# Optimization experiments

Hardware: AMD Instinct MI355X
Metric: run time of the kernel (lower is better)

## Reference

```python
import jax, jax.numpy as jnp
import numpy as np

B, D, K, H, L = 8192, 512, 64, 256, 3  # batch, hidden width, rank_k, hypernet hidden, n layers


def _xavier(key, shape):
    fan_in, fan_out = shape[0], shape[1]
    std = float(np.sqrt(2.0 / (fan_in + fan_out)))
    return jax.random.normal(key, shape, dtype=jnp.float32) * std


def setup_inputs() -> dict:
    key = jax.random.key(0)
    ks = jax.random.split(key, 32)
    inp = {"x": jax.random.normal(ks[0], (B, D), dtype=jnp.float32)}
    i = 1
    for l in range(1, L + 1):
        inp[f"U{l}"] = _xavier(ks[i], (D, K)); i += 1
        inp[f"V{l}"] = _xavier(ks[i], (K, D)); i += 1
        # hypernet: cond_dim D -> H -> (K*K + D) [first D cols are bias]
        inp[f"hW1_{l}"] = _xavier(ks[i], (D, H)); i += 1
        inp[f"hb1_{l}"] = jnp.zeros((H,), dtype=jnp.float32)
        inp[f"hW2_{l}"] = _xavier(ks[i], (H, K * K + D)); i += 1
        inp[f"hb2_{l}"] = jnp.zeros((K * K + D,), dtype=jnp.float32)
    inp["Wout"] = _xavier(ks[i], (D, 1)); i += 1
    inp["bout"] = jnp.zeros((1,), dtype=jnp.float32)
    return inp


def _apg_layer(x, U, V, hW1, hb1, hW2, hb2):
    # hypernet (self-wise: condition_z = x)
    h1 = jax.nn.relu(x @ hW1 + hb1)            # [B, H]
    s = h1 @ hW2 + hb2                          # [B, K*K + D]
    bias = s[:, :D]                             # generated per-sample bias [B, D]
    S = s[:, D:].reshape(-1, K, K)              # per-sample weight [B, K, K]
    h = x @ U                                   # [B, K]
    h = jnp.einsum('bk,bkj->bj', h, S)          # bmm(h.unsqueeze(1), S).squeeze(1)
    out = h @ V + bias                          # [B, D]
    return jax.nn.relu(out)


def reference(x,
              U1, V1, hW1_1, hb1_1, hW2_1, hb2_1,
              U2, V2, hW1_2, hb1_2, hW2_2, hb2_2,
              U3, V3, hW1_3, hb1_3, hW2_3, hb2_3,
              Wout, bout):
    x = _apg_layer(x, U1, V1, hW1_1, hb1_1, hW2_1, hb2_1)
    x = _apg_layer(x, U2, V2, hW1_2, hb1_2, hW2_2, hb2_2)
    x = _apg_layer(x, U3, V3, hW1_3, hb1_3, hW2_3, hb2_3)
    return x @ Wout + bout                      # [B, 1]
```

## Files before the change

kernel.cpp:

```cpp
#include <hip/hip_runtime.h>

#define B_N 8192
#define D_N 512
#define K_N 64
#define H_N 256
#define SC  4608
#define R_T 32
#define NT  512

typedef __attribute__((ext_vector_type(8))) short short8;
typedef __attribute__((ext_vector_type(4))) short short4v;
typedef __attribute__((ext_vector_type(4))) float f32x4;

__device__ __forceinline__ unsigned short f2bf(float f) {
  unsigned int u = __builtin_bit_cast(unsigned int, f);
  u += 0x7fff + ((u >> 16) & 1);
  return (unsigned short)(u >> 16);
}
__device__ __forceinline__ float bf2f(unsigned short h) {
  unsigned int u = ((unsigned int)h) << 16;
  return __builtin_bit_cast(float, u);
}

#define L_ELEMS 1376256

struct PrepParams {
  const float* W1[3]; const float* U[3]; const float* W2[3]; const float* V[3];
  short* ws;
};

__global__ __launch_bounds__(256) void prep_weights(PrepParams p) {
  const int y = blockIdx.y;
  const int l = y / 5, m = y - 5 * l;
  short* wsl = p.ws + (size_t)l * L_ELEMS;
  if (m == 2) {
    const float* in = p.W2[l];
    short* out = wsl + 163840;
    const long total = 1048576;
    for (long e = (long)blockIdx.x * 256 + threadIdx.x; e < total;
         e += (long)gridDim.x * 256) {
      const int te   = (int)(e & 7);
      const int lane = (int)((e >> 3) & 63);
      const int kk   = (int)((e >> 9) & 3);
      const int nq   = (int)((e >> 11) & 3);
      const int h2   = (int)((e >> 13) & 1);
      const int kg   = (int)(e >> 14);
      const int g    = lane >> 4;
      const int l15  = lane & 15;
      const int t    = h2 * 128 + kk * 32 + g * 8 + te;
      out[e] = (short)f2bf(in[(size_t)t * SC + 512 + 64 * kg + nq * 16 + l15]);
    }
    return;
  }
  const float* in; short* out; int K, istride, ioff, kshift;
  switch (m) {
    case 0: in = p.W1[l]; out = wsl;           K = 512; istride = 256;  ioff = 0; kshift = 9; break;
    case 1: in = p.U[l];  out = wsl + 131072;  K = 512; istride = 64;   ioff = 0; kshift = 9; break;
    case 3: in = p.W2[l]; out = wsl + 1212416; K = 256; istride = 4608; ioff = 0; kshift = 8; break;
    default:in = p.V[l];  out = wsl + 1343488; K = 64;  istride = 512;  ioff = 0; kshift = 6; break;
  }
  const long total = (long)K * ((m == 0) ? 256 : (m == 1) ? 64 : 512);
  for (long e = (long)blockIdx.x * 256 + threadIdx.x; e < total;
       e += (long)gridDim.x * 256) {
    const int k = (int)(e & (K - 1));
    const int n = (int)(e >> kshift);
    out[e] = (short)f2bf(in[(size_t)k * istride + ioff + n]);
  }
}

struct Params {
  const float* x;
  const float* b1[3];
  const float* b2[3];
  const float* Wout;
  const float* bout;
  const short* ws;
  float* out;
};

#define XP 520
#define HP 264
#define TP 72

__device__ __forceinline__ void stage_chunk(const short* W2p, short* slotp,
                                            int cglob, int nq, int lane) {
  const short* gp = W2p + (((size_t)cglob * 4 + nq) << 11) + (lane << 3);
#pragma unroll
  for (int i = 0; i < 4; ++i) {
    __builtin_amdgcn_global_load_lds(
        (const __attribute__((address_space(1))) void*)(gp + (i << 9)),
        (__attribute__((address_space(3))) void*)(slotp + (i << 9)), 16, 0, 0);
  }
}

__global__ __launch_bounds__(NT, 1) void apg_mfma(Params p) {
  __shared__ __attribute__((aligned(16))) short ring[8][3][2048];
  __shared__ short h1s[R_T][HP];
  __shared__ short tmps[R_T][TP];
  __shared__ float hs[R_T][68];
  __shared__ float tpart[R_T][68];
  short (*xs)[XP] = (short (*)[XP]) & ring[0][0][0];

  const int tid  = threadIdx.x;
  const int row0 = blockIdx.x * R_T;
  const int w    = tid >> 6;
  const int lane = tid & 63;
  const int l15  = tid & 15;
  const int g    = (tid & 63) >> 4;
  const int koff = g * 8;
  const int rh   = w >> 2;
  const int nq   = w & 3;
  const int rbase = rh * 16;

  {
    const float4* xg = (const float4*)(p.x + (size_t)row0 * D_N);
    for (int i = tid; i < R_T * D_N / 4; i += NT) {
      float4 v = xg[i];
      const int r = i >> 7;
      const int c = (i & 127) << 2;
      short4v s4 = { (short)f2bf(v.x), (short)f2bf(v.y), (short)f2bf(v.z), (short)f2bf(v.w) };
      *(short4v*)&xs[r][c] = s4;
    }
  }
  __syncthreads();

  for (int l = 0; l < 3; ++l) {
    const short* wsl  = p.ws + (size_t)l * L_ELEMS;
    const short* W1T  = wsl;
    const short* UT   = wsl + 131072;
    const short* W2p  = wsl + 163840;
    const short* W2bT = wsl + 1212416;
    const short* VT   = wsl + 1343488;
    const float* b1 = p.b1[l];
    const float* b2 = p.b2[l];

    short8 aX[16];
#pragma unroll
    for (int kk = 0; kk < 16; ++kk)
      aX[kk] = *(const short8*)&xs[rbase + l15][kk * 32 + koff];

    for (int nf = 0; nf < 4; ++nf) {
      const int n0 = ((nq << 2) + nf) << 4;
      const short* pb = W1T + ((size_t)(n0 + l15) << 9) + koff;
      short8 bf[16];
#pragma unroll
      for (int kk = 0; kk < 16; ++kk) bf[kk] = *(const short8*)(pb + kk * 32);
      f32x4 acc = {0.f, 0.f, 0.f, 0.f};
#pragma unroll
      for (int kk = 0; kk < 16; ++kk)
        acc = __builtin_amdgcn_mfma_f32_16x16x32_bf16(aX[kk], bf[kk], acc, 0, 0, 0);
      const float bb = b1[n0 + l15];
#pragma unroll
      for (int i = 0; i < 4; ++i)
        h1s[rbase + g * 4 + i][n0 + l15] = (short)f2bf(fmaxf(acc[i] + bb, 0.f));
    }

    {
      const int n0 = nq << 4;
      const short* pb = UT + ((size_t)(n0 + l15) << 9) + koff;
      short8 bf[16];
#pragma unroll
      for (int kk = 0; kk < 16; ++kk) bf[kk] = *(const short8*)(pb + kk * 32);
      f32x4 acc = {0.f, 0.f, 0.f, 0.f};
#pragma unroll
      for (int kk = 0; kk < 16; ++kk)
        acc = __builtin_amdgcn_mfma_f32_16x16x32_bf16(aX[kk], bf[kk], acc, 0, 0, 0);
#pragma unroll
      for (int i = 0; i < 4; ++i) hs[rbase + g * 4 + i][n0 + l15] = acc[i];
    }
    __syncthreads();

    {
      const int kh  = w >> 2;
      const int kg0 = kh << 5;
      const int nl  = (nq << 4) + l15;
      short8 aH0[8], aH1[8];
#pragma unroll
      for (int kk = 0; kk < 8; ++kk) {
        aH0[kk] = *(const short8*)&h1s[l15][kk * 32 + koff];
        aH1[kk] = *(const short8*)&h1s[16 + l15][kk * 32 + koff];
      }
      float t0[4] = {0.f, 0.f, 0.f, 0.f}, t1[4] = {0.f, 0.f, 0.f, 0.f};
      {
        const float* pb2 = b2 + D_N + nl;
#pragma unroll 4
        for (int k = kg0; k < kg0 + 32; ++k) {
          const float b2v = pb2[k << 6];
#pragma unroll
          for (int i = 0; i < 4; ++i) {
            t0[i] += hs[g * 4 + i][k] * b2v;
            t1[i] += hs[16 + g * 4 + i][k] * b2v;
          }
        }
      }

      short* ringw = &ring[w][0][0];
      const int cbase = kg0 << 1;

      asm volatile("s_waitcnt vmcnt(0)" ::: "memory");
      stage_chunk(W2p, ringw,        cbase + 0, nq, lane);
      stage_chunk(W2p, ringw + 2048, cbase + 1, nq, lane);
      stage_chunk(W2p, ringw + 4096, cbase + 2, nq, lane);

#pragma unroll 1
      for (int kgi = 0; kgi < 32; ++kgi) {
        const int kg = kg0 + kgi;
        f32x4 s0 = {0.f, 0.f, 0.f, 0.f}, s1 = {0.f, 0.f, 0.f, 0.f};
        {
          const int slot = (2 * kgi) % 3;
          if (kgi < 31) asm volatile("s_waitcnt vmcnt(8)" ::: "memory");
          else          asm volatile("s_waitcnt vmcnt(4)" ::: "memory");
          const short* rb = ringw + slot * 2048 + (lane << 3);
          short8 bf[4];
#pragma unroll
          for (int kk = 0; kk < 4; ++kk) bf[kk] = *(const short8*)(rb + (kk << 9));
          asm volatile("s_waitcnt lgkmcnt(0)" ::: "memory");
          __builtin_amdgcn_sched_barrier(0);
          if (kgi <= 30)
            stage_chunk(W2p, ringw + slot * 2048, cbase + 2 * kgi + 3, nq, lane);
#pragma unroll
          for (int kk = 0; kk < 4; ++kk) {
            s0 = __builtin_amdgcn_mfma_f32_16x16x32_bf16(aH0[kk], bf[kk], s0, 0, 0, 0);
            s1 = __builtin_amdgcn_mfma_f32_16x16x32_bf16(aH1[kk], bf[kk], s1, 0, 0, 0);
          }
        }
        {
          const int slot = (2 * kgi + 1) % 3;
          if (kgi < 31) asm volatile("s_waitcnt vmcnt(8)" ::: "memory");
          else          asm volatile("s_waitcnt vmcnt(0)" ::: "memory");
          const short* rb = ringw + slot * 2048 + (lane << 3);
          short8 bf[4];
#pragma unroll
          for (int kk = 0; kk < 4; ++kk) bf[kk] = *(const short8*)(rb + (kk << 9));
          asm volatile("s_waitcnt lgkmcnt(0)" ::: "memory");
          __builtin_amdgcn_sched_barrier(0);
          if (kgi <= 29)
            stage_chunk(W2p, ringw + slot * 2048, cbase + 2 * kgi + 4, nq, lane);
#pragma unroll
          for (int kk = 0; kk < 4; ++kk) {
            s0 = __builtin_amdgcn_mfma_f32_16x16x32_bf16(aH0[4 + kk], bf[kk], s0, 0, 0, 0);
            s1 = __builtin_amdgcn_mfma_f32_16x16x32_bf16(aH1[4 + kk], bf[kk], s1, 0, 0, 0);
          }
        }
#pragma unroll
        for (int i = 0; i < 4; ++i) {
          t0[i] += hs[g * 4 + i][kg] * s0[i];
          t1[i] += hs[16 + g * 4 + i][kg] * s1[i];
        }
      }

      if (kh == 0) {
#pragma unroll
        for (int i = 0; i < 4; ++i) {
          tpart[g * 4 + i][nl]      = t0[i];
          tpart[16 + g * 4 + i][nl] = t1[i];
        }
      }
      __syncthreads();
      if (kh == 1) {
#pragma unroll
        for (int i = 0; i < 4; ++i) {
          tmps[g * 4 + i][nl]      = (short)f2bf(tpart[g * 4 + i][nl] + t0[i]);
          tmps[16 + g * 4 + i][nl] = (short)f2bf(tpart[16 + g * 4 + i][nl] + t1[i]);
        }
      }
    }
    __syncthreads();

    {
      short8 aT[2], aD[8];
#pragma unroll
      for (int kk = 0; kk < 2; ++kk)
        aT[kk] = *(const short8*)&tmps[rbase + l15][kk * 32 + koff];
#pragma unroll
      for (int kk = 0; kk < 8; ++kk)
        aD[kk] = *(const short8*)&h1s[rbase + l15][kk * 32 + koff];
      for (int ti = 0; ti < 8; ++ti) {
        const int n0 = ((ti << 2) + nq) << 4;
        const short* pv = VT + ((size_t)(n0 + l15) << 6) + koff;
        const short* pw = W2bT + ((size_t)(n0 + l15) << 8) + koff;
        short8 bv[2], bw[8];
#pragma unroll
        for (int kk = 0; kk < 2; ++kk) bv[kk] = *(const short8*)(pv + kk * 32);
#pragma unroll
        for (int kk = 0; kk < 8; ++kk) bw[kk] = *(const short8*)(pw + kk * 32);
        f32x4 acc = {0.f, 0.f, 0.f, 0.f};
#pragma unroll
        for (int kk = 0; kk < 2; ++kk)
          acc = __builtin_amdgcn_mfma_f32_16x16x32_bf16(aT[kk], bv[kk], acc, 0, 0, 0);
#pragma unroll
        for (int kk = 0; kk < 8; ++kk)
          acc = __builtin_amdgcn_mfma_f32_16x16x32_bf16(aD[kk], bw[kk], acc, 0, 0, 0);
        const float bb = b2[n0 + l15];
#pragma unroll
        for (int i = 0; i < 4; ++i)
          xs[rbase + g * 4 + i][n0 + l15] = (short)f2bf(fmaxf(acc[i] + bb, 0.f));
      }
    }
    __syncthreads();
  }

  {
    const int r  = tid >> 4;
    const int cl = tid & 15;
    float acc = 0.f;
    for (int c = cl; c < D_N; c += 16)
      acc = fmaf(bf2f((unsigned short)xs[r][c]), p.Wout[c], acc);
#pragma unroll
    for (int s = 1; s < 16; s <<= 1) acc += __shfl_xor(acc, s, 64);
    if (cl == 0) p.out[row0 + r] = acc + p.bout[0];
  }
}

extern "C" void kernel_launch(void* const* d_in, const int* in_sizes, int n_in,
                              void* d_out, int out_size, void* d_ws, size_t ws_size,
                              hipStream_t stream) {
  (void)in_sizes; (void)n_in; (void)ws_size; (void)out_size;
  PrepParams pp;
  Params p;
  p.x = (const float*)d_in[0];
  for (int l = 0; l < 3; ++l) {
    const int base = 1 + l * 6;
    pp.U[l]  = (const float*)d_in[base + 0];
    pp.V[l]  = (const float*)d_in[base + 1];
    pp.W1[l] = (const float*)d_in[base + 2];
    p.b1[l]  = (const float*)d_in[base + 3];
    pp.W2[l] = (const float*)d_in[base + 4];
    p.b2[l]  = (const float*)d_in[base + 5];
  }
  p.Wout = (const float*)d_in[19];
  p.bout = (const float*)d_in[20];
  p.ws   = (const short*)d_ws;
  p.out  = (float*)d_out;
  pp.ws  = (short*)d_ws;

  hipLaunchKernelGGL(prep_weights, dim3(1024, 15), dim3(256), 0, stream, pp);
  hipLaunchKernelGGL(apg_mfma, dim3(B_N / R_T), dim3(NT), 0, stream, p);
}
```

Before: 216.3 us.

## Split fused APG layer kernel into per-stage kernels with workspace intermediates

Replaces the single fused per-row-tile kernel with a multi-kernel pipeline per layer: one kernel computes h1 and x@U, one computes the per-sample einsum with 64-row tiles split across two blocks per tile and combined by atomicAdd into a zeroed fp32 buffer, and one computes the V projection plus generated bias, with a final output kernel. Intermediates go through global workspace instead of LDS, and the W2 weight layout is repacked for the new einsum tiling. The intent is to raise parallelism and weight reuse in the dominant einsum stage, at the cost of extra launches, memsets, global round-trips and atomics. The old fused path is kept as a fallback when the workspace is too small.

```diff
diff --git a/kernel.cpp b/kernel.cpp
--- a/kernel.cpp
+++ b/kernel.cpp
@@ -5,7 +5,6 @@
 #define K_N 64
 #define H_N 256
 #define SC  4608
-#define R_T 32
 #define NT  512
 
 typedef __attribute__((ext_vector_type(8))) short short8;
@@ -24,12 +23,262 @@
 
 #define L_ELEMS 1376256
 
+#define OFF_H1  8257536u
+#define OFF_H   12451840u
+#define OFF_TMP 14548992u
+#define OFF_X   16646144u
+#define WS_NEED 25034752u
+
 struct PrepParams {
   const float* W1[3]; const float* U[3]; const float* W2[3]; const float* V[3];
   short* ws;
 };
 
-__global__ __launch_bounds__(256) void prep_weights(PrepParams p) {
+__global__ __launch_bounds__(256) void prep_main(PrepParams p) {
+  const int y = blockIdx.y;
+  const int l = y / 5, m = y - 5 * l;
+  short* wsl = p.ws + (size_t)l * L_ELEMS;
+  if (m == 2) {
+    const float* in = p.W2[l];
+    short* out = wsl + 163840;
+    const long total = 1048576;
+    for (long e = (long)blockIdx.x * 256 + threadIdx.x; e < total;
+         e += (long)gridDim.x * 256) {
+      const int te   = (int)(e & 7);
+      const int lane = (int)((e >> 3) & 63);
+      const int cf   = (int)((e >> 9) & 3);
+      const int ks   = (int)((e >> 11) & 7);
+      const int kg   = (int)(e >> 14);
+      const int t    = ks * 32 + (lane >> 4) * 8 + te;
+      const int j    = cf * 16 + (lane & 15);
+      out[e] = (short)f2bf(in[(size_t)t * SC + 512 + 64 * kg + j]);
+    }
+    return;
+  }
+  const float* in; short* out; int K, istride, ioff, kshift;
+  switch (m) {
+    case 0: in = p.W1[l]; out = wsl;           K = 512; istride = 256;  ioff = 0; kshift = 9; break;
+    case 1: in = p.U[l];  out = wsl + 131072;  K = 512; istride = 64;   ioff = 0; kshift = 9; break;
+    case 3: in = p.W2[l]; out = wsl + 1212416; K = 256; istride = 4608; ioff = 0; kshift = 8; break;
+    default:in = p.V[l];  out = wsl + 1343488; K = 64;  istride = 512;  ioff = 0; kshift = 6; break;
+  }
+  const long total = (long)K * ((m == 0) ? 256 : (m == 1) ? 64 : 512);
+  for (long e = (long)blockIdx.x * 256 + threadIdx.x; e < total;
+       e += (long)gridDim.x * 256) {
+    const int k = (int)(e & (K - 1));
+    const int n = (int)(e >> kshift);
+    out[e] = (short)f2bf(in[(size_t)k * istride + ioff + n]);
+  }
+}
+
+struct K1Params {
+  const float* xf;
+  const short* xb;
+  const short* wsl;
+  const float* b1;
+  short* h1w; float* hw;
+};
+__global__ __launch_bounds__(NT, 1) void k1_h1h(K1Params p) {
+  __shared__ short xs[32][520];
+  const int tid = threadIdx.x;
+  const int w = tid >> 6, rh = w >> 2, nq = w & 3;
+  const int l15 = tid & 15, g = (tid & 63) >> 4, koff = g * 8;
+  const int R0 = blockIdx.x * 32, rbase = rh * 16;
+
+  if (p.xf) {
+    const float4* xg = (const float4*)(p.xf + (size_t)R0 * D_N);
+    for (int i = tid; i < 32 * D_N / 4; i += NT) {
+      float4 v = xg[i];
+      const int r = i >> 7, c = (i & 127) << 2;
+      short4v s4 = { (short)f2bf(v.x), (short)f2bf(v.y), (short)f2bf(v.z), (short)f2bf(v.w) };
+      *(short4v*)&xs[r][c] = s4;
+    }
+  } else {
+    const short8* xg = (const short8*)(p.xb + (size_t)R0 * D_N);
+    for (int i = tid; i < 32 * D_N / 8; i += NT) {
+      short8 v = xg[i];
+      const int r = i >> 6, c = (i & 63) << 3;
+      *(short8*)&xs[r][c] = v;
+    }
+  }
+  __syncthreads();
+
+  short8 aX[16];
+#pragma unroll
+  for (int kk = 0; kk < 16; ++kk)
+    aX[kk] = *(const short8*)&xs[rbase + l15][kk * 32 + koff];
+
+  for (int f = 0; f < 5; ++f) {
+    const int n0 = nq * 80 + f * 16;
+    const bool ish1 = (n0 < 256);
+    const short* pb = ish1 ? (p.wsl + ((size_t)(n0 + l15) << 9) + koff)
+                           : (p.wsl + 131072 + ((size_t)(n0 - 256 + l15) << 9) + koff);
+    short8 bf[16];
+#pragma unroll
+    for (int kk = 0; kk < 16; ++kk) bf[kk] = *(const short8*)(pb + kk * 32);
+    f32x4 acc = {0.f, 0.f, 0.f, 0.f};
+#pragma unroll
+    for (int kk = 0; kk < 16; ++kk)
+      acc = __builtin_amdgcn_mfma_f32_16x16x32_bf16(aX[kk], bf[kk], acc, 0, 0, 0);
+    if (ish1) {
+      const float bb = p.b1[n0 + l15];
+#pragma unroll
+      for (int i = 0; i < 4; ++i)
+        p.h1w[(size_t)(R0 + rbase + g * 4 + i) * 256 + n0 + l15] =
+            (short)f2bf(fmaxf(acc[i] + bb, 0.f));
+    } else {
+#pragma unroll
+      for (int i = 0; i < 4; ++i)
+        p.hw[(size_t)(R0 + rbase + g * 4 + i) * 64 + (n0 - 256) + l15] = acc[i];
+    }
+  }
+}
+
+struct K2Params {
+  const short* w2k; const short* h1w; const float* hw;
+  const float* b2; float* tmpf;
+};
+__global__ __launch_bounds__(NT, 1) void k2_einsum(K2Params p) {
+  __shared__ float tpartL[4][64][68];
+  const int tid = threadIdx.x;
+  const int w = tid >> 6, lane = tid & 63;
+  const int l15 = tid & 15, g = (tid & 63) >> 4, koff = g * 8;
+  const int rt = blockIdx.x >> 1, kh = blockIdx.x & 1;
+  const int R0 = rt * 64;
+  const int m2 = w >> 2, s = w & 3;
+  const int rb = m2 * 32;
+  const int kgbase = kh * 32 + s * 8;
+
+  short8 aH0[8], aH1[8];
+#pragma unroll
+  for (int kk = 0; kk < 8; ++kk) {
+    aH0[kk] = *(const short8*)&p.h1w[(size_t)(R0 + rb + l15) * 256 + kk * 32 + koff];
+    aH1[kk] = *(const short8*)&p.h1w[(size_t)(R0 + rb + 16 + l15) * 256 + kk * 32 + koff];
+  }
+  float ta0[4][4] = {{0.f}}, ta1[4][4] = {{0.f}};
+
+#pragma unroll 1
+  for (int q = 0; q < 8; ++q) {
+    const int kg = kgbase + q;
+    const short* bbase = p.w2k + ((size_t)kg << 14) + (lane << 3);
+    f32x4 s0[4], s1[4];
+#pragma unroll
+    for (int cf = 0; cf < 4; ++cf) {
+      f32x4 z = {0.f, 0.f, 0.f, 0.f};
+      s0[cf] = z; s1[cf] = z;
+    }
+#pragma unroll
+    for (int h2 = 0; h2 < 2; ++h2) {
+      short8 bf[16];
+#pragma unroll
+      for (int kw = 0; kw < 4; ++kw)
+#pragma unroll
+        for (int cf = 0; cf < 4; ++cf)
+          bf[kw * 4 + cf] = *(const short8*)(bbase + ((((h2 * 4 + kw) * 4 + cf)) << 9));
+#pragma unroll
+      for (int kw = 0; kw < 4; ++kw)
+#pragma unroll
+        for (int cf = 0; cf < 4; ++cf) {
+          s0[cf] = __builtin_amdgcn_mfma_f32_16x16x32_bf16(aH0[h2 * 4 + kw], bf[kw * 4 + cf], s0[cf], 0, 0, 0);
+          s1[cf] = __builtin_amdgcn_mfma_f32_16x16x32_bf16(aH1[h2 * 4 + kw], bf[kw * 4 + cf], s1[cf], 0, 0, 0);
+        }
+    }
+    const float* pb2 = p.b2 + D_N + (kg << 6);
+    float b2v[4];
+#pragma unroll
+    for (int cf = 0; cf < 4; ++cf) b2v[cf] = pb2[cf * 16 + l15];
+#pragma unroll
+    for (int i = 0; i < 4; ++i) {
+      const float hv0 = p.hw[(size_t)(R0 + rb + g * 4 + i) * 64 + kg];
+      const float hv1 = p.hw[(size_t)(R0 + rb + 16 + g * 4 + i) * 64 + kg];
+#pragma unroll
+      for (int cf = 0; cf < 4; ++cf) {
+        ta0[cf][i] += hv0 * (s0[cf][i] + b2v[cf]);
+        ta1[cf][i] += hv1 * (s1[cf][i] + b2v[cf]);
+      }
+    }
+  }
+
+#pragma unroll
+  for (int cf = 0; cf < 4; ++cf)
+#pragma unroll
+    for (int i = 0; i < 4; ++i) {
+      tpartL[s][rb + g * 4 + i][cf * 16 + l15]      = ta0[cf][i];
+      tpartL[s][rb + 16 + g * 4 + i][cf * 16 + l15] = ta1[cf][i];
+    }
+  __syncthreads();
+  for (int e = tid; e < 4096; e += NT) {
+    const int r = e >> 6, c = e & 63;
+    const float v = (tpartL[0][r][c] + tpartL[1][r][c]) +
+                    (tpartL[2][r][c] + tpartL[3][r][c]);
+    atomicAdd(&p.tmpf[(size_t)(R0 + r) * 64 + c], v);
+  }
+}
+
+struct K3Params {
+  const short* wsl; const short* h1w; const float* tmpf;
+  const float* b2; short* xw;
+};
+__global__ __launch_bounds__(NT, 1) void k3_proj(K3Params p) {
+  const int tid = threadIdx.x;
+  const int w = tid >> 6, rh = w >> 2, nq = w & 3;
+  const int l15 = tid & 15, g = (tid & 63) >> 4, koff = g * 8;
+  const int R0 = blockIdx.x * 32, rbase = rh * 16;
+  const short* W2bT = p.wsl + 1212416;
+  const short* VT   = p.wsl + 1343488;
+
+  short8 aT[2];
+#pragma unroll
+  for (int kk = 0; kk < 2; ++kk) {
+    short8 t;
+#pragma unroll
+    for (int e = 0; e < 8; ++e)
+      t[e] = (short)f2bf(p.tmpf[(size_t)(R0 + rbase + l15) * 64 + kk * 32 + koff + e]);
+    aT[kk] = t;
+  }
+  short8 aD[8];
+#pragma unroll
+  for (int kk = 0; kk < 8; ++kk)
+    aD[kk] = *(const short8*)&p.h1w[(size_t)(R0 + rbase + l15) * 256 + kk * 32 + koff];
+
+  for (int ti = 0; ti < 8; ++ti) {
+    const int n0 = ((ti << 2) + nq) << 4;
+    const short* pv = VT + ((size_t)(n0 + l15) << 6) + koff;
+    const short* pw = W2bT + ((size_t)(n0 + l15) << 8) + koff;
+    short8 bv[2], bw[8];
+#pragma unroll
+    for (int kk = 0; kk < 2; ++kk) bv[kk] = *(const short8*)(pv + kk * 32);
+#pragma unroll
+    for (int kk = 0; kk < 8; ++kk) bw[kk] = *(const short8*)(pw + kk * 32);
+    f32x4 acc = {0.f, 0.f, 0.f, 0.f};
+#pragma unroll
+    for (int kk = 0; kk < 2; ++kk)
+      acc = __builtin_amdgcn_mfma_f32_16x16x32_bf16(aT[kk], bv[kk], acc, 0, 0, 0);
+#pragma unroll
+    for (int kk = 0; kk < 8; ++kk)
+      acc = __builtin_amdgcn_mfma_f32_16x16x32_bf16(aD[kk], bw[kk], acc, 0, 0, 0);
+    const float bb = p.b2[n0 + l15];
+#pragma unroll
+    for (int i = 0; i < 4; ++i)
+      p.xw[(size_t)(R0 + rbase + g * 4 + i) * 512 + n0 + l15] =
+          (short)f2bf(fmaxf(acc[i] + bb, 0.f));
+  }
+}
+
+__global__ __launch_bounds__(NT, 1) void k4_out(const short* xw, const float* Wout,
+                                                const float* bout, float* out) {
+  const int tid = threadIdx.x;
+  const int R0 = blockIdx.x * 32;
+  const int r = tid >> 4, cl = tid & 15;
+  float acc = 0.f;
+  for (int c = cl; c < D_N; c += 16)
+    acc = fmaf(bf2f((unsigned short)xw[(size_t)(R0 + r) * 512 + c]), Wout[c], acc);
+#pragma unroll
+  for (int s = 1; s < 16; s <<= 1) acc += __shfl_xor(acc, s, 64);
+  if (cl == 0) out[R0 + r] = acc + bout[0];
+}
+
+__global__ __launch_bounds__(256) void prep_fb(PrepParams p) {
   const int y = blockIdx.y;
   const int l = y / 5, m = y - 5 * l;
   short* wsl = p.ws + (size_t)l * L_ELEMS;
@@ -93,16 +342,16 @@
   }
 }
 
-__global__ __launch_bounds__(NT, 1) void apg_mfma(Params p) {
+__global__ __launch_bounds__(NT, 1) void apg_fb(Params p) {
   __shared__ __attribute__((aligned(16))) short ring[8][3][2048];
-  __shared__ short h1s[R_T][HP];
-  __shared__ short tmps[R_T][TP];
-  __shared__ float hs[R_T][68];
-  __shared__ float tpart[R_T][68];
+  __shared__ short h1s[32][HP];
+  __shared__ short tmps[32][TP];
+  __shared__ float hs[32][68];
+  __shared__ float tpart[32][68];
   short (*xs)[XP] = (short (*)[XP]) & ring[0][0][0];
 
   const int tid  = threadIdx.x;
-  const int row0 = blockIdx.x * R_T;
+  const int row0 = blockIdx.x * 32;
   const int w    = tid >> 6;
   const int lane = tid & 63;
   const int l15  = tid & 15;
@@ -114,7 +363,7 @@
 
   {
     const float4* xg = (const float4*)(p.x + (size_t)row0 * D_N);
-    for (int i = tid; i < R_T * D_N / 4; i += NT) {
+    for (int i = tid; i < 32 * D_N / 4; i += NT) {
       float4 v = xg[i];
       const int r = i >> 7;
       const int c = (i & 127) << 2;
@@ -315,25 +564,61 @@
 extern "C" void kernel_launch(void* const* d_in, const int* in_sizes, int n_in,
                               void* d_out, int out_size, void* d_ws, size_t ws_size,
                               hipStream_t stream) {
-  (void)in_sizes; (void)n_in; (void)ws_size; (void)out_size;
+  (void)in_sizes; (void)n_in; (void)out_size;
   PrepParams pp;
-  Params p;
-  p.x = (const float*)d_in[0];
+  const float* xf = (const float*)d_in[0];
+  const float* b1p[3]; const float* b2p[3];
   for (int l = 0; l < 3; ++l) {
     const int base = 1 + l * 6;
     pp.U[l]  = (const float*)d_in[base + 0];
     pp.V[l]  = (const float*)d_in[base + 1];
     pp.W1[l] = (const float*)d_in[base + 2];
-    p.b1[l]  = (const float*)d_in[base + 3];
+    b1p[l]   = (const float*)d_in[base + 3];
     pp.W2[l] = (const float*)d_in[base + 4];
-    p.b2[l]  = (const float*)d_in[base + 5];
-  }
-  p.Wout = (const float*)d_in[19];
-  p.bout = (const float*)d_in[20];
-  p.ws   = (const short*)d_ws;
-  p.out  = (float*)d_out;
-  pp.ws  = (short*)d_ws;
-
-  hipLaunchKernelGGL(prep_weights, dim3(1024, 15), dim3(256), 0, stream, pp);
-  hipLaunchKernelGGL(apg_mfma, dim3(B_N / R_T), dim3(NT), 0, stream, p);
-}
+    b2p[l]   = (const float*)d_in[base + 5];
+  }
+  const float* Wout = (const float*)d_in[19];
+  const float* bout = (const float*)d_in[20];
+  pp.ws = (short*)d_ws;
+
+  if (ws_size >= (size_t)WS_NEED) {
+    short* wsw  = (short*)d_ws;
+    short* h1w  = (short*)((char*)d_ws + OFF_H1);
+    float* hw   = (float*)((char*)d_ws + OFF_H);
+    float* tmpf = (float*)((char*)d_ws + OFF_TMP);
+    short* xw   = (short*)((char*)d_ws + OFF_X);
+
+    hipLaunchKernelGGL(prep_main, dim3(1024, 15), dim3(256), 0, stream, pp);
+    for (int l = 0; l < 3; ++l) {
+      K1Params p1;
+      p1.xf = (l == 0) ? xf : nullptr;
+      p1.xb = xw;
+      p1.wsl = wsw + (size_t)l * L_ELEMS;
+      p1.b1 = b1p[l]; p1.h1w = h1w; p1.hw = hw;
+      hipLaunchKernelGGL(k1_h1h, dim3(B_N / 32), dim3(NT), 0, stream, p1);
+
+      hipMemsetAsync(tmpf, 0, (size_t)B_N * 64 * 4, stream);
+
+      K2Params p2;
+      p2.w2k = wsw + (size_t)l * L_ELEMS + 163840;
+      p2.h1w = h1w; p2.hw = hw; p2.b2 = b2p[l]; p2.tmpf = tmpf;
+      hipLaunchKernelGGL(k2_einsum, dim3(B_N / 32), dim3(NT), 0, stream, p2);
+
+      K3Params p3;
+      p3.wsl = wsw + (size_t)l * L_ELEMS;
+      p3.h1w = h1w; p3.tmpf = tmpf; p3.b2 = b2p[l]; p3.xw = xw;
+      hipLaunchKernelGGL(k3_proj, dim3(B_N / 32), dim3(NT), 0, stream, p3);
+    }
+    hipLaunchKernelGGL(k4_out, dim3(B_N / 32), dim3(NT), 0, stream,
+                       (const short*)xw, Wout, bout, (float*)d_out);
+  } else {
+    Params p;
+    p.x = xf;
+    for (int l = 0; l < 3; ++l) { p.b1[l] = b1p[l]; p.b2[l] = b2p[l]; }
+    p.Wout = Wout; p.bout = bout;
+    p.ws = (const short*)d_ws;
+    p.out = (float*)d_out;
+    hipLaunchKernelGGL(prep_fb, dim3(1024, 15), dim3(256), 0, stream, pp);
+    hipLaunchKernelGGL(apg_fb, dim3(B_N / 32), dim3(NT), 0, stream, p);
+  }
+}
```

Result: slower. 351.1 us (+62.3%).

## Split fused APG kernel into per-layer kernels with 64-row tiles and split-K atomics

Applied to the files above, without the earlier changes.

The single fused three-layer kernel becomes three launches per layer plus a final output kernel. The hypernet stage now works on 64-row tiles, so each W2 chunk streamed into LDS is reused across four 16-row MFMA sets instead of two. The K-group dimension is split across two blocks that merge partial results with global float atomics into a zeroed buffer. The cost is extra launches and memsets, global round trips for h1, the partial results and x between kernels, and atomic traffic.

```diff
diff --git a/kernel.cpp b/kernel.cpp
--- a/kernel.cpp
+++ b/kernel.cpp
@@ -5,7 +5,6 @@
 #define K_N 64
 #define H_N 256
 #define SC  4608
-#define R_T 32
 #define NT  512
 
 typedef __attribute__((ext_vector_type(8))) short short8;
@@ -23,6 +22,10 @@
 }
 
 #define L_ELEMS 1376256
+
+#define OFF_H1  8257536u
+#define OFF_TMP 14548992u
+#define OFF_X   16646144u
 
 struct PrepParams {
   const float* W1[3]; const float* U[3]; const float* W2[3]; const float* V[3];
@@ -68,20 +71,6 @@
   }
 }
 
-struct Params {
-  const float* x;
-  const float* b1[3];
-  const float* b2[3];
-  const float* Wout;
-  const float* bout;
-  const short* ws;
-  float* out;
-};
-
-#define XP 520
-#define HP 264
-#define TP 72
-
 __device__ __forceinline__ void stage_chunk(const short* W2p, short* slotp,
                                             int cglob, int nq, int lane) {
   const short* gp = W2p + (((size_t)cglob * 4 + nq) << 11) + (lane << 3);
@@ -93,247 +82,312 @@
   }
 }
 
-__global__ __launch_bounds__(NT, 1) void apg_mfma(Params p) {
+struct PParams {
+  const float* xf;
+  const short* xb;
+  const short* wsl;
+  const float* b1;
+  const float* b2;
+  short* h1w;
+  float* tmpf;
+};
+
+__global__ __launch_bounds__(NT, 1) void apg_p(PParams p) {
   __shared__ __attribute__((aligned(16))) short ring[8][3][2048];
-  __shared__ short h1s[R_T][HP];
-  __shared__ short tmps[R_T][TP];
-  __shared__ float hs[R_T][68];
-  __shared__ float tpart[R_T][68];
-  short (*xs)[XP] = (short (*)[XP]) & ring[0][0][0];
+  __shared__ short h1s[64][264];
+  __shared__ float hs[64][68];
+  short (*xs)[520] = (short (*)[520]) & ring[0][0][0];
 
   const int tid  = threadIdx.x;
-  const int row0 = blockIdx.x * R_T;
   const int w    = tid >> 6;
   const int lane = tid & 63;
   const int l15  = tid & 15;
   const int g    = (tid & 63) >> 4;
   const int koff = g * 8;
-  const int rh   = w >> 2;
   const int nq   = w & 3;
-  const int rbase = rh * 16;
-
-  {
-    const float4* xg = (const float4*)(p.x + (size_t)row0 * D_N);
-    for (int i = tid; i < R_T * D_N / 4; i += NT) {
+  const int rt   = blockIdx.x >> 1;
+  const int kh   = blockIdx.x & 1;
+  const int R0   = rt * 64;
+
+  if (p.xf) {
+    const float4* xg = (const float4*)(p.xf + (size_t)R0 * D_N);
+    for (int i = tid; i < 64 * D_N / 4; i += NT) {
       float4 v = xg[i];
-      const int r = i >> 7;
-      const int c = (i & 127) << 2;
+      const int r = i >> 7, c = (i & 127) << 2;
       short4v s4 = { (short)f2bf(v.x), (short)f2bf(v.y), (short)f2bf(v.z), (short)f2bf(v.w) };
       *(short4v*)&xs[r][c] = s4;
     }
+  } else {
+    const short8* xg = (const short8*)(p.xb + (size_t)R0 * D_N);
+    for (int i = tid; i < 64 * D_N / 8; i += NT) {
+      short8 v = xg[i];
+      const int r = i >> 6, c = (i & 63) << 3;
+      *(short8*)&xs[r][c] = v;
+    }
   }
   __syncthreads();
 
-  for (int l = 0; l < 3; ++l) {
-    const short* wsl  = p.ws + (size_t)l * L_ELEMS;
-    const short* W1T  = wsl;
-    const short* UT   = wsl + 131072;
-    const short* W2p  = wsl + 163840;
-    const short* W2bT = wsl + 1212416;
-    const short* VT   = wsl + 1343488;
-    const float* b1 = p.b1[l];
-    const float* b2 = p.b2[l];
-
-    short8 aX[16];
-#pragma unroll
-    for (int kk = 0; kk < 16; ++kk)
-      aX[kk] = *(const short8*)&xs[rbase + l15][kk * 32 + koff];
-
-    for (int nf = 0; nf < 4; ++nf) {
-      const int n0 = ((nq << 2) + nf) << 4;
-      const short* pb = W1T + ((size_t)(n0 + l15) << 9) + koff;
-      short8 bf[16];
-#pragma unroll
-      for (int kk = 0; kk < 16; ++kk) bf[kk] = *(const short8*)(pb + kk * 32);
-      f32x4 acc = {0.f, 0.f, 0.f, 0.f};
+  {
+    const int rh2 = w >> 2;
+    for (int rs = 0; rs < 2; ++rs) {
+      const int rb = rh2 * 32 + rs * 16;
+      short8 aX[16];
 #pragma unroll
       for (int kk = 0; kk < 16; ++kk)
-        acc = __builtin_amdgcn_mfma_f32_16x16x32_bf16(aX[kk], bf[kk], acc, 0, 0, 0);
-      const float bb = b1[n0 + l15];
-#pragma unroll
-      for (int i = 0; i < 4; ++i)
-        h1s[rbase + g * 4 + i][n0 + l15] = (short)f2bf(fmaxf(acc[i] + bb, 0.f));
-    }
-
+        aX[kk] = *(const short8*)&xs[rb + l15][kk * 32 + koff];
+      for (int f = 0; f < 5; ++f) {
+        const int n0 = nq * 80 + f * 16;
+        const bool ish1 = (n0 < 256);
+        const short* pb = ish1 ? (p.wsl + ((size_t)(n0 + l15) << 9) + koff)
+                               : (p.wsl + 131072 + ((size_t)(n0 - 256 + l15) << 9) + koff);
+        short8 bf[16];
+#pragma unroll
+        for (int kk = 0; kk < 16; ++kk) bf[kk] = *(const short8*)(pb + kk * 32);
+        f32x4 acc = {0.f, 0.f, 0.f, 0.f};
+#pragma unroll
+        for (int kk = 0; kk < 16; ++kk)
+          acc = __builtin_amdgcn_mfma_f32_16x16x32_bf16(aX[kk], bf[kk], acc, 0, 0, 0);
+        if (ish1) {
+          const float bb = p.b1[n0 + l15];
+#pragma unroll
+          for (int i = 0; i < 4; ++i) {
+            const short v = (short)f2bf(fmaxf(acc[i] + bb, 0.f));
+            h1s[rb + g * 4 + i][n0 + l15] = v;
+            if (kh == 0)
+              p.h1w[(size_t)(R0 + rb + g * 4 + i) * 256 + n0 + l15] = v;
+          }
+        } else {
+#pragma unroll
+          for (int i = 0; i < 4; ++i)
+            hs[rb + g * 4 + i][n0 - 256 + l15] = acc[i];
+        }
+      }
+    }
+  }
+  __syncthreads();
+
+  {
+    const short* W2p = p.wsl + 163840;
+    const int kq   = w >> 2;
+    const int kg0w = kh * 32 + kq * 16;
+    const int nl   = nq * 16 + l15;
+    float t[4][4];
+#pragma unroll
+    for (int rset = 0; rset < 4; ++rset)
+#pragma unroll
+      for (int i = 0; i < 4; ++i) t[rset][i] = 0.f;
     {
-      const int n0 = nq << 4;
-      const short* pb = UT + ((size_t)(n0 + l15) << 9) + koff;
-      short8 bf[16];
-#pragma unroll
-      for (int kk = 0; kk < 16; ++kk) bf[kk] = *(const short8*)(pb + kk * 32);
-      f32x4 acc = {0.f, 0.f, 0.f, 0.f};
-#pragma unroll
-      for (int kk = 0; kk < 16; ++kk)
-        acc = __builtin_amdgcn_mfma_f32_16x16x32_bf16(aX[kk], bf[kk], acc, 0, 0, 0);
-#pragma unroll
-      for (int i = 0; i < 4; ++i) hs[rbase + g * 4 + i][n0 + l15] = acc[i];
+      const float* pb2 = p.b2 + D_N + nl;
+#pragma unroll 4
+      for (int k = kg0w; k < kg0w + 16; ++k) {
+        const float b2v = pb2[k << 6];
+#pragma unroll
+        for (int rset = 0; rset < 4; ++rset)
+#pragma unroll
+          for (int i = 0; i < 4; ++i)
+            t[rset][i] += hs[rset * 16 + g * 4 + i][k] * b2v;
+      }
+    }
+
+    short* ringw = &ring[w][0][0];
+    const int cbase = kg0w << 1;
+
+    asm volatile("s_waitcnt vmcnt(0)" ::: "memory");
+    stage_chunk(W2p, ringw,        cbase + 0, nq, lane);
+    stage_chunk(W2p, ringw + 2048, cbase + 1, nq, lane);
+    stage_chunk(W2p, ringw + 4096, cbase + 2, nq, lane);
+
+#pragma unroll 1
+    for (int kgi = 0; kgi < 16; ++kgi) {
+      const int kg = kg0w + kgi;
+      f32x4 s[4];
+#pragma unroll
+      for (int rset = 0; rset < 4; ++rset) {
+        f32x4 z = {0.f, 0.f, 0.f, 0.f};
+        s[rset] = z;
+      }
+      {
+        const int slot = (2 * kgi) % 3;
+        if (kgi < 15) asm volatile("s_waitcnt vmcnt(8)" ::: "memory");
+        else          asm volatile("s_waitcnt vmcnt(4)" ::: "memory");
+        const short* rb = ringw + slot * 2048 + (lane << 3);
+        short8 bf[4];
+#pragma unroll
+        for (int kk = 0; kk < 4; ++kk) bf[kk] = *(const short8*)(rb + (kk << 9));
+        short8 aHt[4][4];
+#pragma unroll
+        for (int rset = 0; rset < 4; ++rset)
+#pragma unroll
+          for (int kk = 0; kk < 4; ++kk)
+            aHt[rset][kk] = *(const short8*)&h1s[rset * 16 + l15][kk * 32 + koff];
+        asm volatile("s_waitcnt lgkmcnt(0)" ::: "memory");
+        __builtin_amdgcn_sched_barrier(0);
+        if (2 * kgi + 3 <= 31)
+          stage_chunk(W2p, ringw + slot * 2048, cbase + 2 * kgi + 3, nq, lane);
+#pragma unroll
+        for (int kk = 0; kk < 4; ++kk)
+#pragma unroll
+          for (int rset = 0; rset < 4; ++rset)
+            s[rset] = __builtin_amdgcn_mfma_f32_16x16x32_bf16(aHt[rset][kk], bf[kk], s[rset], 0, 0, 0);
+      }
+      {
+        const int slot = (2 * kgi + 1) % 3;
+        if (kgi < 15) asm volatile("s_waitcnt vmcnt(8)" ::: "memory");
+        else          asm volatile("s_waitcnt vmcnt(0)" ::: "memory");
+        const short* rb = ringw + slot * 2048 + (lane << 3);
+        short8 bf[4];
+#pragma unroll
+        for (int kk = 0; kk < 4; ++kk) bf[kk] = *(const short8*)(rb + (kk << 9));
+        short8 aHt[4][4];
+#pragma unroll
+        for (int rset = 0; rset < 4; ++rset)
+#pragma unroll
+          for (int kk = 0; kk < 4; ++kk)
+            aHt[rset][kk] = *(const short8*)&h1s[rset * 16 + l15][(4 + kk) * 32 + koff];
+        asm volatile("s_waitcnt lgkmcnt(0)" ::: "memory");
+        __builtin_amdgcn_sched_barrier(0);
+        if (2 * kgi + 4 <= 31)
+          stage_chunk(W2p, ringw + slot * 2048, cbase + 2 * kgi + 4, nq, lane);
+#pragma unroll
+        for (int kk = 0; kk < 4; ++kk)
+#pragma unroll
+          for (int rset = 0; rset < 4; ++rset)
+            s[rset] = __builtin_amdgcn_mfma_f32_16x16x32_bf16(aHt[rset][kk], bf[kk], s[rset], 0, 0, 0);
+      }
+#pragma unroll
+      for (int rset = 0; rset < 4; ++rset)
+#pragma unroll
+        for (int i = 0; i < 4; ++i)
+          t[rset][i] += hs[rset * 16 + g * 4 + i][kg] * s[rset][i];
+    }
+
+    float* tpw = (float*)&ring[w][0][0];
+    if (kq == 0) {
+#pragma unroll
+      for (int rset = 0; rset < 4; ++rset)
+#pragma unroll
+        for (int i = 0; i < 4; ++i)
+          tpw[(rset * 16 + g * 4 + i) * 16 + l15] = t[rset][i];
     }
     __syncthreads();
-
-    {
-      const int kh  = w >> 2;
-      const int kg0 = kh << 5;
-      const int nl  = (nq << 4) + l15;
-      short8 aH0[8], aH1[8];
-#pragma unroll
-      for (int kk = 0; kk < 8; ++kk) {
-        aH0[kk] = *(const short8*)&h1s[l15][kk * 32 + koff];
-        aH1[kk] = *(const short8*)&h1s[16 + l15][kk * 32 + koff];
-      }
-      float t0[4] = {0.f, 0.f, 0.f, 0.f}, t1[4] = {0.f, 0.f, 0.f, 0.f};
-      {
-        const float* pb2 = b2 + D_N + nl;
-#pragma unroll 4
-        for (int k = kg0; k < kg0 + 32; ++k) {
-          const float b2v = pb2[k << 6];
-#pragma unroll
-          for (int i = 0; i < 4; ++i) {
-            t0[i] += hs[g * 4 + i][k] * b2v;
-            t1[i] += hs[16 + g * 4 + i][k] * b2v;
-          }
+    if (kq == 1) {
+      const float* tpp = (const float*)&ring[nq][0][0];
+#pragma unroll
+      for (int rset = 0; rset < 4; ++rset)
+#pragma unroll
+        for (int i = 0; i < 4; ++i) {
+          const int row = rset * 16 + g * 4 + i;
+          const float v = tpp[row * 16 + l15] + t[rset][i];
+          atomicAdd(&p.tmpf[(size_t)(R0 + row) * 64 + nl], v);
         }
-      }
-
-      short* ringw = &ring[w][0][0];
-      const int cbase = kg0 << 1;
-
-      asm volatile("s_waitcnt vmcnt(0)" ::: "memory");
-      stage_chunk(W2p, ringw,        cbase + 0, nq, lane);
-      stage_chunk(W2p, ringw + 2048, cbase + 1, nq, lane);
-      stage_chunk(W2p, ringw + 4096, cbase + 2, nq, lane);
-
-#pragma unroll 1
-      for (int kgi = 0; kgi < 32; ++kgi) {
-        const int kg = kg0 + kgi;
-        f32x4 s0 = {0.f, 0.f, 0.f, 0.f}, s1 = {0.f, 0.f, 0.f, 0.f};
-        {
-          const int slot = (2 * kgi) % 3;
-          if (kgi < 31) asm volatile("s_waitcnt vmcnt(8)" ::: "memory");
-          else          asm volatile("s_waitcnt vmcnt(4)" ::: "memory");
-          const short* rb = ringw + slot * 2048 + (lane << 3);
-          short8 bf[4];
-#pragma unroll
-          for (int kk = 0; kk < 4; ++kk) bf[kk] = *(const short8*)(rb + (kk << 9));
-          asm volatile("s_waitcnt lgkmcnt(0)" ::: "memory");
-          __builtin_amdgcn_sched_barrier(0);
-          if (kgi <= 30)
-            stage_chunk(W2p, ringw + slot * 2048, cbase + 2 * kgi + 3, nq, lane);
-#pragma unroll
-          for (int kk = 0; kk < 4; ++kk) {
-            s0 = __builtin_amdgcn_mfma_f32_16x16x32_bf16(aH0[kk], bf[kk], s0, 0, 0, 0);
-            s1 = __builtin_amdgcn_mfma_f32_16x16x32_bf16(aH1[kk], bf[kk], s1, 0, 0, 0);
-          }
-        }
-        {
-          const int slot = (2 * kgi + 1) % 3;
-          if (kgi < 31) asm volatile("s_waitcnt vmcnt(8)" ::: "memory");
-          else          asm volatile("s_waitcnt vmcnt(0)" ::: "memory");
-          const short* rb = ringw + slot * 2048 + (lane << 3);
-          short8 bf[4];
-#pragma unroll
-          for (int kk = 0; kk < 4; ++kk) bf[kk] = *(const short8*)(rb + (kk << 9));
-          asm volatile("s_waitcnt lgkmcnt(0)" ::: "memory");
-          __builtin_amdgcn_sched_barrier(0);
-          if (kgi <= 29)
-            stage_chunk(W2p, ringw + slot * 2048, cbase + 2 * kgi + 4, nq, lane);
-#pragma unroll
-          for (int kk = 0; kk < 4; ++kk) {
-            s0 = __builtin_amdgcn_mfma_f32_16x16x32_bf16(aH0[4 + kk], bf[kk], s0, 0, 0, 0);
-            s1 = __builtin_amdgcn_mfma_f32_16x16x32_bf16(aH1[4 + kk], bf[kk], s1, 0, 0, 0);
-          }
-        }
-#pragma unroll
-        for (int i = 0; i < 4; ++i) {
-          t0[i] += hs[g * 4 + i][kg] * s0[i];
-          t1[i] += hs[16 + g * 4 + i][kg] * s1[i];
-        }
-      }
-
-      if (kh == 0) {
-#pragma unroll
-        for (int i = 0; i < 4; ++i) {
-          tpart[g * 4 + i][nl]      = t0[i];
-          tpart[16 + g * 4 + i][nl] = t1[i];
-        }
-      }
-      __syncthreads();
-      if (kh == 1) {
-#pragma unroll
-        for (int i = 0; i < 4; ++i) {
-          tmps[g * 4 + i][nl]      = (short)f2bf(tpart[g * 4 + i][nl] + t0[i]);
-          tmps[16 + g * 4 + i][nl] = (short)f2bf(tpart[16 + g * 4 + i][nl] + t1[i]);
-        }
-      }
-    }
-    __syncthreads();
-
-    {
-      short8 aT[2], aD[8];
-#pragma unroll
-      for (int kk = 0; kk < 2; ++kk)
-        aT[kk] = *(const short8*)&tmps[rbase + l15][kk * 32 + koff];
-#pragma unroll
-      for (int kk = 0; kk < 8; ++kk)
-        aD[kk] = *(const short8*)&h1s[rbase + l15][kk * 32 + koff];
-      for (int ti = 0; ti < 8; ++ti) {
-        const int n0 = ((ti << 2) + nq) << 4;
-        const short* pv = VT + ((size_t)(n0 + l15) << 6) + koff;
-        const short* pw = W2bT + ((size_t)(n0 + l15) << 8) + koff;
-        short8 bv[2], bw[8];
-#pragma unroll
-        for (int kk = 0; kk < 2; ++kk) bv[kk] = *(const short8*)(pv + kk * 32);
-#pragma unroll
-        for (int kk = 0; kk < 8; ++kk) bw[kk] = *(const short8*)(pw + kk * 32);
-        f32x4 acc = {0.f, 0.f, 0.f, 0.f};
-#pragma unroll
-        for (int kk = 0; kk < 2; ++kk)
-          acc = __builtin_amdgcn_mfma_f32_16x16x32_bf16(aT[kk], bv[kk], acc, 0, 0, 0);
-#pragma unroll
-        for (int kk = 0; kk < 8; ++kk)
-          acc = __builtin_amdgcn_mfma_f32_16x16x32_bf16(aD[kk], bw[kk], acc, 0, 0, 0);
-        const float bb = b2[n0 + l15];
-#pragma unroll
-        for (int i = 0; i < 4; ++i)
-          xs[rbase + g * 4 + i][n0 + l15] = (short)f2bf(fmaxf(acc[i] + bb, 0.f));
-      }
-    }
-    __syncthreads();
-  }
-
-  {
-    const int r  = tid >> 4;
-    const int cl = tid & 15;
-    float acc = 0.f;
-    for (int c = cl; c < D_N; c += 16)
-      acc = fmaf(bf2f((unsigned short)xs[r][c]), p.Wout[c], acc);
-#pragma unroll
-    for (int s = 1; s < 16; s <<= 1) acc += __shfl_xor(acc, s, 64);
-    if (cl == 0) p.out[row0 + r] = acc + p.bout[0];
-  }
+    }
+  }
+}
+
+struct K3Params {
+  const short* wsl; const short* h1w; const float* tmpf;
+  const float* b2; short* xw;
+};
+__global__ __launch_bounds__(NT, 1) void k3_proj(K3Params p) {
+  const int tid = threadIdx.x;
+  const int w = tid >> 6, rh = w >> 2, nq = w & 3;
+  const int l15 = tid & 15, g = (tid & 63) >> 4, koff = g * 8;
+  const int R0 = blockIdx.x * 32, rbase = rh * 16;
+  const short* W2bT = p.wsl + 1212416;
+  const short* VT   = p.wsl + 1343488;
+
+  short8 aT[2];
+#pragma unroll
+  for (int kk = 0; kk < 2; ++kk) {
+    short8 t;
+#pragma unroll
+    for (int e = 0; e < 8; ++e)
+      t[e] = (short)f2bf(p.tmpf[(size_t)(R0 + rbase + l15) * 64 + kk * 32 + koff + e]);
+    aT[kk] = t;
+  }
+  short8 aD[8];
+#pragma unroll
+  for (int kk = 0; kk < 8; ++kk)
+    aD[kk] = *(const short8*)&p.h1w[(size_t)(R0 + rbase + l15) * 256 + kk * 32 + koff];
+
+  for (int ti = 0; ti < 8; ++ti) {
+    const int n0 = ((ti << 2) + nq) << 4;
+    const short* pv = VT + ((size_t)(n0 + l15) << 6) + koff;
+    const short* pw = W2bT + ((size_t)(n0 + l15) << 8) + koff;
+    short8 bv[2], bw[8];
+#pragma unroll
+    for (int kk = 0; kk < 2; ++kk) bv[kk] = *(const short8*)(pv + kk * 32);
+#pragma unroll
+    for (int kk = 0; kk < 8; ++kk) bw[kk] = *(const short8*)(pw + kk * 32);
+    f32x4 acc = {0.f, 0.f, 0.f, 0.f};
+#pragma unroll
+    for (int kk = 0; kk < 2; ++kk)
+      acc = __builtin_amdgcn_mfma_f32_16x16x32_bf16(aT[kk], bv[kk], acc, 0, 0, 0);
+#pragma unroll
+    for (int kk = 0; kk < 8; ++kk)
+      acc = __builtin_amdgcn_mfma_f32_16x16x32_bf16(aD[kk], bw[kk], acc, 0, 0, 0);
+    const float bb = p.b2[n0 + l15];
+#pragma unroll
+    for (int i = 0; i < 4; ++i)
+      p.xw[(size_t)(R0 + rbase + g * 4 + i) * 512 + n0 + l15] =
+          (short)f2bf(fmaxf(acc[i] + bb, 0.f));
+  }
+}
+
+__global__ __launch_bounds__(NT, 1) void k4_out(const short* xw, const float* Wout,
+                                                const float* bout, float* out) {
+  const int tid = threadIdx.x;
+  const int R0 = blockIdx.x * 32;
+  const int r = tid >> 4, cl = tid & 15;
+  float acc = 0.f;
+  for (int c = cl; c < D_N; c += 16)
+    acc = fmaf(bf2f((unsigned short)xw[(size_t)(R0 + r) * 512 + c]), Wout[c], acc);
+#pragma unroll
+  for (int s = 1; s < 16; s <<= 1) acc += __shfl_xor(acc, s, 64);
+  if (cl == 0) out[R0 + r] = acc + bout[0];
 }
 
 extern "C" void kernel_launch(void* const* d_in, const int* in_sizes, int n_in,
                               void* d_out, int out_size, void* d_ws, size_t ws_size,
                               hipStream_t stream) {
-  (void)in_sizes; (void)n_in; (void)ws_size; (void)out_size;
+  (void)in_sizes; (void)n_in; (void)out_size; (void)ws_size;
   PrepParams pp;
-  Params p;
-  p.x = (const float*)d_in[0];
+  const float* xf = (const float*)d_in[0];
+  const float* b1p[3]; const float* b2p[3];
   for (int l = 0; l < 3; ++l) {
     const int base = 1 + l * 6;
     pp.U[l]  = (const float*)d_in[base + 0];
     pp.V[l]  = (const float*)d_in[base + 1];
     pp.W1[l] = (const float*)d_in[base + 2];
-    p.b1[l]  = (const float*)d_in[base + 3];
+    b1p[l]   = (const float*)d_in[base + 3];
     pp.W2[l] = (const float*)d_in[base + 4];
-    p.b2[l]  = (const float*)d_in[base + 5];
-  }
-  p.Wout = (const float*)d_in[19];
-  p.bout = (const float*)d_in[20];
-  p.ws   = (const short*)d_ws;
-  p.out  = (float*)d_out;
-  pp.ws  = (short*)d_ws;
+    b2p[l]   = (const float*)d_in[base + 5];
+  }
+  const float* Wout = (const float*)d_in[19];
+  const float* bout = (const float*)d_in[20];
+  pp.ws = (short*)d_ws;
+
+  short* wsw  = (short*)d_ws;
+  short* h1w  = (short*)((char*)d_ws + OFF_H1);
+  float* tmpf = (float*)((char*)d_ws + OFF_TMP);
+  short* xw   = (short*)((char*)d_ws + OFF_X);
 
   hipLaunchKernelGGL(prep_weights, dim3(1024, 15), dim3(256), 0, stream, pp);
-  hipLaunchKernelGGL(apg_mfma, dim3(B_N / R_T), dim3(NT), 0, stream, p);
-}
+  for (int l = 0; l < 3; ++l) {
+    hipMemsetAsync(tmpf, 0, (size_t)B_N * 64 * 4, stream);
+    PParams p1;
+    p1.xf = (l == 0) ? xf : nullptr;
+    p1.xb = xw;
+    p1.wsl = wsw + (size_t)l * L_ELEMS;
+    p1.b1 = b1p[l]; p1.b2 = b2p[l];
+    p1.h1w = h1w; p1.tmpf = tmpf;
+    hipLaunchKernelGGL(apg_p, dim3(B_N / 32), dim3(NT), 0, stream, p1);
+
+    K3Params p3;
+    p3.wsl = wsw + (size_t)l * L_ELEMS;
+    p3.h1w = h1w; p3.tmpf = tmpf; p3.b2 = b2p[l]; p3.xw = xw;
+    hipLaunchKernelGGL(k3_proj, dim3(B_N / 32), dim3(NT), 0, stream, p3);
+  }
+  hipLaunchKernelGGL(k4_out, dim3(B_N / 32), dim3(NT), 0, stream,
+                     (const short*)xw, Wout, bout, (float*)d_out);
+}
```

Measured after the change: 316.0 us. 46.1% more time.

## Deepen W2 LDS ring to four slots with register double-buffered B fragments

Applied to the files above, without the earlier changes.

Grows the per-wave LDS ring from three to four chunk slots and restructures the main loop into a 4-chunk unrolled software pipeline. Each chunk's LDS reads are issued one stage ahead, into alternating register buffers, so they overlap with the MFMAs of the previous chunk instead of waiting on lgkmcnt(0). The tpart reduction buffer is removed and the ring memory is reused for the cross-wave partial sums, which offsets the LDS growth. This adds register pressure and complexity in the waitcnt accounting.

```diff
diff --git a/kernel.cpp b/kernel.cpp
--- a/kernel.cpp
+++ b/kernel.cpp
@@ -93,12 +93,45 @@
   }
 }
 
+#define DS_READ4(dst, SLOT)                                                   \
+  do {                                                                        \
+    const short* rb_ = ringw + (SLOT) * 2048 + (lane << 3);                   \
+    dst[0] = *(const short8*)(rb_);                                           \
+    dst[1] = *(const short8*)(rb_ + 512);                                     \
+    dst[2] = *(const short8*)(rb_ + 1024);                                    \
+    dst[3] = *(const short8*)(rb_ + 1536);                                    \
+  } while (0)
+
+#define MFMA_TH0(bf)                                                          \
+  do {                                                                        \
+    f32x4 z_ = {0.f, 0.f, 0.f, 0.f};                                          \
+    s0 = z_; s1 = z_;                                                         \
+    _Pragma("unroll")                                                         \
+    for (int kk = 0; kk < 4; ++kk) {                                          \
+      s0 = __builtin_amdgcn_mfma_f32_16x16x32_bf16(aH0[kk], bf[kk], s0, 0, 0, 0); \
+      s1 = __builtin_amdgcn_mfma_f32_16x16x32_bf16(aH1[kk], bf[kk], s1, 0, 0, 0); \
+    }                                                                         \
+  } while (0)
+
+#define MFMA_TH1_FOLD(bf, KG)                                                 \
+  do {                                                                        \
+    _Pragma("unroll")                                                         \
+    for (int kk = 0; kk < 4; ++kk) {                                          \
+      s0 = __builtin_amdgcn_mfma_f32_16x16x32_bf16(aH0[4 + kk], bf[kk], s0, 0, 0, 0); \
+      s1 = __builtin_amdgcn_mfma_f32_16x16x32_bf16(aH1[4 + kk], bf[kk], s1, 0, 0, 0); \
+    }                                                                         \
+    _Pragma("unroll")                                                         \
+    for (int i = 0; i < 4; ++i) {                                             \
+      t0[i] += hs[g * 4 + i][(KG)] * s0[i];                                   \
+      t1[i] += hs[16 + g * 4 + i][(KG)] * s1[i];                              \
+    }                                                                         \
+  } while (0)
+
 __global__ __launch_bounds__(NT, 1) void apg_mfma(Params p) {
-  __shared__ __attribute__((aligned(16))) short ring[8][3][2048];
+  __shared__ __attribute__((aligned(16))) short ring[8][4][2048];
   __shared__ short h1s[R_T][HP];
   __shared__ short tmps[R_T][TP];
   __shared__ float hs[R_T][68];
-  __shared__ float tpart[R_T][68];
   short (*xs)[XP] = (short (*)[XP]) & ring[0][0][0];
 
   const int tid  = threadIdx.x;
@@ -201,67 +234,76 @@
       stage_chunk(W2p, ringw,        cbase + 0, nq, lane);
       stage_chunk(W2p, ringw + 2048, cbase + 1, nq, lane);
       stage_chunk(W2p, ringw + 4096, cbase + 2, nq, lane);
+      stage_chunk(W2p, ringw + 6144, cbase + 3, nq, lane);
+      asm volatile("s_waitcnt vmcnt(12)" ::: "memory");
+      short8 bfA[4], bfB[4];
+      DS_READ4(bfA, 0);
+      f32x4 s0, s1;
 
 #pragma unroll 1
-      for (int kgi = 0; kgi < 32; ++kgi) {
-        const int kg = kg0 + kgi;
-        f32x4 s0 = {0.f, 0.f, 0.f, 0.f}, s1 = {0.f, 0.f, 0.f, 0.f};
-        {
-          const int slot = (2 * kgi) % 3;
-          if (kgi < 31) asm volatile("s_waitcnt vmcnt(8)" ::: "memory");
-          else          asm volatile("s_waitcnt vmcnt(4)" ::: "memory");
-          const short* rb = ringw + slot * 2048 + (lane << 3);
-          short8 bf[4];
-#pragma unroll
-          for (int kk = 0; kk < 4; ++kk) bf[kk] = *(const short8*)(rb + (kk << 9));
-          asm volatile("s_waitcnt lgkmcnt(0)" ::: "memory");
-          __builtin_amdgcn_sched_barrier(0);
-          if (kgi <= 30)
-            stage_chunk(W2p, ringw + slot * 2048, cbase + 2 * kgi + 3, nq, lane);
-#pragma unroll
-          for (int kk = 0; kk < 4; ++kk) {
-            s0 = __builtin_amdgcn_mfma_f32_16x16x32_bf16(aH0[kk], bf[kk], s0, 0, 0, 0);
-            s1 = __builtin_amdgcn_mfma_f32_16x16x32_bf16(aH1[kk], bf[kk], s1, 0, 0, 0);
-          }
-        }
-        {
-          const int slot = (2 * kgi + 1) % 3;
-          if (kgi < 31) asm volatile("s_waitcnt vmcnt(8)" ::: "memory");
-          else          asm volatile("s_waitcnt vmcnt(0)" ::: "memory");
-          const short* rb = ringw + slot * 2048 + (lane << 3);
-          short8 bf[4];
-#pragma unroll
-          for (int kk = 0; kk < 4; ++kk) bf[kk] = *(const short8*)(rb + (kk << 9));
-          asm volatile("s_waitcnt lgkmcnt(0)" ::: "memory");
-          __builtin_amdgcn_sched_barrier(0);
-          if (kgi <= 29)
-            stage_chunk(W2p, ringw + slot * 2048, cbase + 2 * kgi + 4, nq, lane);
-#pragma unroll
-          for (int kk = 0; kk < 4; ++kk) {
-            s0 = __builtin_amdgcn_mfma_f32_16x16x32_bf16(aH0[4 + kk], bf[kk], s0, 0, 0, 0);
-            s1 = __builtin_amdgcn_mfma_f32_16x16x32_bf16(aH1[4 + kk], bf[kk], s1, 0, 0, 0);
-          }
-        }
+      for (int it = 0; it < 15; ++it) {
+        const int c0 = it << 2;
+        asm volatile("s_waitcnt vmcnt(8)" ::: "memory");
+        DS_READ4(bfB, 1);
+        asm volatile("s_waitcnt lgkmcnt(4)" ::: "memory");
+        __builtin_amdgcn_sched_barrier(0);
+        MFMA_TH0(bfA);
+        stage_chunk(W2p, ringw,        cbase + c0 + 4, nq, lane);
+        asm volatile("s_waitcnt vmcnt(8)" ::: "memory");
+        DS_READ4(bfA, 2);
+        asm volatile("s_waitcnt lgkmcnt(4)" ::: "memory");
+        __builtin_amdgcn_sched_barrier(0);
+        MFMA_TH1_FOLD(bfB, kg0 + 2 * it);
+        stage_chunk(W2p, ringw + 2048, cbase + c0 + 5, nq, lane);
+        asm volatile("s_waitcnt vmcnt(8)" ::: "memory");
+        DS_READ4(bfB, 3);
+        asm volatile("s_waitcnt lgkmcnt(4)" ::: "memory");
+        __builtin_amdgcn_sched_barrier(0);
+        MFMA_TH0(bfA);
+        stage_chunk(W2p, ringw + 4096, cbase + c0 + 6, nq, lane);
+        asm volatile("s_waitcnt vmcnt(8)" ::: "memory");
+        DS_READ4(bfA, 0);
+        asm volatile("s_waitcnt lgkmcnt(4)" ::: "memory");
+        __builtin_amdgcn_sched_barrier(0);
+        MFMA_TH1_FOLD(bfB, kg0 + 2 * it + 1);
+        stage_chunk(W2p, ringw + 6144, cbase + c0 + 7, nq, lane);
+      }
+      asm volatile("s_waitcnt vmcnt(8)" ::: "memory");
+      DS_READ4(bfB, 1);
+      asm volatile("s_waitcnt lgkmcnt(4)" ::: "memory");
+      __builtin_amdgcn_sched_barrier(0);
+      MFMA_TH0(bfA);
+      asm volatile("s_waitcnt vmcnt(4)" ::: "memory");
+      DS_READ4(bfA, 2);
+      asm volatile("s_waitcnt lgkmcnt(4)" ::: "memory");
+      __builtin_amdgcn_sched_barrier(0);
+      MFMA_TH1_FOLD(bfB, kg0 + 30);
+      asm volatile("s_waitcnt vmcnt(0)" ::: "memory");
+      DS_READ4(bfB, 3);
+      asm volatile("s_waitcnt lgkmcnt(4)" ::: "memory");
+      __builtin_amdgcn_sched_barrier(0);
+      MFMA_TH0(bfA);
+      asm volatile("s_waitcnt lgkmcnt(0)" ::: "memory");
+      __builtin_amdgcn_sched_barrier(0);
+      MFMA_TH1_FOLD(bfB, kg0 + 31);
+
+      float* tpw = (float*)&ring[w][0][0];
+      if (kh == 0) {
 #pragma unroll
         for (int i = 0; i < 4; ++i) {
-          t0[i] += hs[g * 4 + i][kg] * s0[i];
-          t1[i] += hs[16 + g * 4 + i][kg] * s1[i];
-        }
-      }
-
-      if (kh == 0) {
-#pragma unroll
-        for (int i = 0; i < 4; ++i) {
-          tpart[g * 4 + i][nl]      = t0[i];
-          tpart[16 + g * 4 + i][nl] = t1[i];
+          tpw[(g * 4 + i) * 16 + l15]        = t0[i];
+          tpw[(16 + g * 4 + i) * 16 + l15]   = t1[i];
         }
       }
       __syncthreads();
       if (kh == 1) {
+        const float* tpp = (const float*)&ring[w - 4][0][0];
 #pragma unroll
         for (int i = 0; i < 4; ++i) {
-          tmps[g * 4 + i][nl]      = (short)f2bf(tpart[g * 4 + i][nl] + t0[i]);
-          tmps[16 + g * 4 + i][nl] = (short)f2bf(tpart[16 + g * 4 + i][nl] + t1[i]);
+          tmps[g * 4 + i][nl] =
+              (short)f2bf(tpp[(g * 4 + i) * 16 + l15] + t0[i]);
+          tmps[16 + g * 4 + i][nl] =
+              (short)f2bf(tpp[(16 + g * 4 + i) * 16 + l15] + t1[i]);
         }
       }
     }
```

Result: faster. 194.9 us (median of 2 runs) (-9.9%).
